# Kernel tuning notes

Hardware: AMD Instinct MI355X
Metric: run time of the kernel (lower is better)

## Reference

```python
import jax, jax.numpy as jnp
import numpy as np

N = 100000      # nodes
E = 800000      # edges (nnz of sparse adj)
D_IN = 128      # input feature dim
H = 64          # hidden_units
EMB = 32        # embsize
N_IDX = 50000   # gathered output rows
EPS = 1e-05     # BatchNormalization epsilon


def spmm(rows, cols, vals, x):
    # out[i] = sum_{e: rows[e]==i} vals[e] * x[cols[e]]  == sparse A @ x
    return jax.ops.segment_sum(vals[:, None] * x[cols], rows, num_segments=N)


def batchnorm(x, gamma, beta):
    # training-mode BN over node (batch) axis, matching Keras BatchNormalization
    m = jnp.mean(x, axis=0)
    v = jnp.var(x, axis=0)
    return (x - m) * jax.lax.rsqrt(v + EPS) * gamma + beta


def setup_inputs() -> dict:
    key = jax.random.key(0)
    ks = jax.random.split(key, 16)
    def w(k, fan_in, shape):
        return jax.random.normal(k, shape, dtype=jnp.float32) / np.sqrt(fan_in)
    inp = {
        "features": jax.random.normal(ks[0], (N, D_IN), dtype=jnp.float32),
        "rows": jax.random.randint(ks[1], (E,), 0, N),
        "cols": jax.random.randint(ks[2], (E,), 0, N),
        "vals": jax.random.uniform(ks[3], (E,), dtype=jnp.float32),
        "idx": jax.random.randint(ks[4], (N_IDX,), 0, N),
        # layer 0 (Dense with bias since l==0)
        "Wn0": w(ks[5], D_IN, (D_IN, H)), "bn0": jnp.zeros((H,), jnp.float32),
        "Wg0": w(ks[6], D_IN, (D_IN, H)), "bg0": jnp.zeros((H,), jnp.float32),
        "ab0": jnp.zeros((H,), jnp.float32),  # BiasLayer after SpMM
        "g0": jnp.ones((H,), jnp.float32), "b0": jnp.zeros((H,), jnp.float32),
        # layer 1 (no Dense bias)
        "Wn1": w(ks[7], H, (H, H)),
        "Wg1": w(ks[8], H, (H, H)),
        "ab1": jnp.zeros((H,), jnp.float32),
        "g1": jnp.ones((H,), jnp.float32), "b1": jnp.zeros((H,), jnp.float32),
        # conv_last block (Dense use_bias=False)
        "WnL": w(ks[9], H, (H, EMB)),
        "WgL": w(ks[10], H, (H, EMB)),
        "abL": jnp.zeros((EMB,), jnp.float32),
    }
    return inp


def reference(features, rows, cols, vals, idx,
              Wn0, bn0, Wg0, bg0, ab0, g0, b0,
              Wn1, Wg1, ab1, g1, b1,
              WnL, WgL, abL):
    x = features
    # SAGE layer 0
    x_node = x @ Wn0 + bn0
    x_neigh = x @ Wg0 + bg0
    agg = spmm(rows, cols, vals, x_neigh) + ab0
    x = jax.nn.relu(batchnorm(x_node + agg, g0, b0))
    # SAGE layer 1
    x_node = x @ Wn1
    x_neigh = x @ Wg1
    agg = spmm(rows, cols, vals, x_neigh) + ab1
    x = jax.nn.relu(batchnorm(x_node + agg, g1, b1))
    # conv_last projection to embsize
    x_node = x @ WnL
    x_neigh = x @ WgL
    agg = spmm(rows, cols, vals, x_neigh) + abL
    x = x_node + agg
    return x[idx]
```

## Files before the change

### kernel.cpp

```cpp
#include <hip/hip_runtime.h>

#define NNODES 100000
#define NEDGES 800000
#define DIN    128
#define HID    64
#define EMB    32
#define NIDX   50000
#define BN_EPS 1e-5f

#define NCHK 256
#define EC   (NEDGES / NCHK)
#define SUBC 256
#define ECS  (NEDGES / SUBC)
#define NB   ((NNODES + 63) / 64)
#define HB   ((NB + 1) / 2)

typedef __attribute__((ext_vector_type(8))) short short8;
typedef __attribute__((ext_vector_type(4))) float f32x4;

__device__ inline unsigned short f2bf(float f) {
    unsigned u = __float_as_uint(f);
    unsigned r = u + 0x7FFFu + ((u >> 16) & 1u);
    return (unsigned short)(r >> 16);
}
__device__ inline float bf2f_lo(unsigned u) { return __uint_as_float(u << 16); }
__device__ inline float bf2f_hi(unsigned u) { return __uint_as_float(u & 0xffff0000u); }


__device__ inline void pack_seg(const float* __restrict__ Wn, const float* __restrict__ Wg,
                                unsigned short* __restrict__ Wp, int HOUT, int l2nt, int f) {
    int j = f & 7, lane = (f >> 3) & 63, g = f >> 9;
    int tt = g & ((1 << l2nt) - 1), kb = g >> l2nt;
    int k = kb * 32 + ((lane >> 4) * 8) + j;
    int nn = tt * 16 + (lane & 15);
    float v = (nn < HOUT) ? Wn[k * HOUT + nn] : Wg[k * HOUT + (nn - HOUT)];
    Wp[f] = f2bf(v);
}


__global__ __launch_bounds__(256) void histpack_k(
    const int* __restrict__ rows, int* __restrict__ Bcnt4,
    const int* __restrict__ idx, int* __restrict__ mark,
    const float* Wn0, const float* Wg0, const float* Wn1,
    const float* Wg1, const float* WnL, const float* WgL,
    unsigned short* Wp0, unsigned short* Wp1, unsigned short* WpL, int MB)
{
    int blk = blockIdx.x;
    if (blk >= SUBC + MB) {
        int f = (blk - SUBC - MB) * 256 + threadIdx.x;
        if (f < 16384)      pack_seg(Wn0, Wg0, Wp0, 64, 3, f);
        else if (f < 24576) pack_seg(Wn1, Wg1, Wp1, 64, 3, f - 16384);
        else if (f < 28672) pack_seg(WnL, WgL, WpL, 32, 2, f - 24576);
        return;
    }
    if (blk >= SUBC) {
        int j = (blk - SUBC) * 256 + threadIdx.x;
        if (j < NIDX) mark[idx[j]] = 1;
        return;
    }
    __shared__ int hist[NB];
    int t = threadIdx.x;
    for (int b = t; b < NB; b += 256) hist[b] = 0;
    __syncthreads();
    for (int i = t; i < ECS; i += 256)
        atomicAdd(&hist[rows[blk * ECS + i] >> 6], 1);
    __syncthreads();
    for (int b = t; b < NB; b += 256) Bcnt4[blk * NB + b] = hist[b];
}

__global__ void bprefix_k(const int* __restrict__ Bcnt4, int* __restrict__ BcntT,
                          int* __restrict__ bTot) {
    int b = blockIdx.x * 256 + threadIdx.x;
    if (b >= NB) return;
    int run = 0;
    for (int sub = 0; sub < SUBC; sub++) {
        BcntT[sub * NB + b] = run;
        run += Bcnt4[sub * NB + b];
    }
    bTot[b] = run;
}

__global__ void bscan_k(const int* __restrict__ bTot, int* __restrict__ bBase) {
    __shared__ int s[256];
    int t = threadIdx.x;
    int v[7], loc = 0;
#pragma unroll
    for (int i = 0; i < 7; i++) {
        int ix = t * 7 + i;
        v[i] = loc;
        loc += (ix < NB) ? bTot[ix] : 0;
    }
    s[t] = loc;
    __syncthreads();
    for (int off = 1; off < 256; off <<= 1) {
        int a = (t >= off) ? s[t - off] : 0;
        __syncthreads();
        s[t] += a;
        __syncthreads();
    }
    int base = s[t] - loc;
#pragma unroll
    for (int i = 0; i < 7; i++) {
        int ix = t * 7 + i;
        if (ix < NB) bBase[ix] = base + v[i];
    }
    if (t == 255) bBase[NB] = NEDGES;
}

__global__ __launch_bounds__(256) void bfinal_k(const uint2* __restrict__ ebuf,
                                                const int* __restrict__ bBase,
                                                int* __restrict__ rowptr,
                                                int2* __restrict__ cs) {
    __shared__ int hist[64], sc[64], cur[64];
    int b = blockIdx.x, t = threadIdx.x;
    int e0 = bBase[b], e1 = bBase[b + 1];
    int r0 = b << 6;
    if (t < 64) hist[t] = 0;
    __syncthreads();
    for (int i = e0 + t; i < e1; i += 256)
        atomicAdd(&hist[(ebuf[i].x >> 20) & 63], 1);
    __syncthreads();
    if (t == 0) {
        int run = e0;
        for (int j = 0; j < 64; j++) { sc[j] = run; run += hist[j]; }
    }
    __syncthreads();
    if (t < 64) {
        cur[t] = sc[t];
        int r = r0 + t;
        if (r < NNODES) rowptr[r] = sc[t];
    }
    if (b == NB - 1 && t == 0) rowptr[NNODES] = NEDGES;
    __syncthreads();
    for (int i = e0 + t; i < e1; i += 256) {
        uint2 v = ebuf[i];
        int p = atomicAdd(&cur[(v.x >> 20) & 63], 1);
        cs[p] = make_int2((int)(v.x & 0xFFFFF), (int)v.y);
    }
}


template <int K, int HOUT, bool AFF, bool XBF, bool HNBF>
__device__ void gemm_body(const void* __restrict__ Xv, const unsigned short* __restrict__ Wp,
                          const float* __restrict__ bnA, const float* __restrict__ bnB,
                          const float* __restrict__ bgA,
                          const float* __restrict__ sums, const float* __restrict__ gamma,
                          const float* __restrict__ beta,
                          float* __restrict__ Hnf, unsigned short* __restrict__ Hnb,
                          unsigned short* __restrict__ Hgb, int n, int blk)
{
    constexpr int NT = 2 * HOUT / 16, NKB = K / 32;
    constexpr int RS = K + 8;
    __shared__ unsigned short Xs[64 * RS];
    __shared__ float sSc[64], sSh[64];

    const int row0 = blk * 64;
    const int t = threadIdx.x;

    if (AFF) {
        if (t < 64) {
            float sum = 0.f, sq = 0.f;
#pragma unroll
            for (int s = 0; s < 8; s++) { sum += sums[s * 128 + t]; sq += sums[s * 128 + 64 + t]; }
            float m = sum / (float)NNODES;
            float var = sq / (float)NNODES - m * m;
            float sc = gamma[t] * rsqrtf(var + BN_EPS);
            sSc[t] = sc; sSh[t] = beta[t] - m * sc;
        }
        __syncthreads();
    }

    for (int li = t; li < 64 * K / 8; li += 256) {
        int r  = li / (K / 8);
        int k8 = (li % (K / 8)) * 8;
        int rr = row0 + r;
        float v[8];
        if (XBF) {
            uint4 u = (rr < n) ? *(const uint4*)((const unsigned short*)Xv + (size_t)rr * K + k8)
                               : make_uint4(0, 0, 0, 0);
            v[0] = bf2f_lo(u.x); v[1] = bf2f_hi(u.x);
            v[2] = bf2f_lo(u.y); v[3] = bf2f_hi(u.y);
            v[4] = bf2f_lo(u.z); v[5] = bf2f_hi(u.z);
            v[6] = bf2f_lo(u.w); v[7] = bf2f_hi(u.w);
        } else {
            const float* Xf = (const float*)Xv;
            float4 a = make_float4(0.f, 0.f, 0.f, 0.f), b = a;
            if (rr < n) {
                a = *(const float4*)&Xf[(size_t)rr * K + k8];
                b = *(const float4*)&Xf[(size_t)rr * K + k8 + 4];
            }
            v[0] = a.x; v[1] = a.y; v[2] = a.z; v[3] = a.w;
            v[4] = b.x; v[5] = b.y; v[6] = b.z; v[7] = b.w;
        }
        if (AFF) {
#pragma unroll
            for (int i = 0; i < 8; i++) v[i] = fmaxf(v[i] * sSc[k8 + i] + sSh[k8 + i], 0.f);
        }
        uint4 o;
        o.x = (unsigned)f2bf(v[0]) | ((unsigned)f2bf(v[1]) << 16);
        o.y = (unsigned)f2bf(v[2]) | ((unsigned)f2bf(v[3]) << 16);
        o.z = (unsigned)f2bf(v[4]) | ((unsigned)f2bf(v[5]) << 16);
        o.w = (unsigned)f2bf(v[6]) | ((unsigned)f2bf(v[7]) << 16);
        *(uint4*)&Xs[r * RS + k8] = o;
    }
    __syncthreads();

    const int wave = t >> 6, lane = t & 63;
    const int q = lane >> 4, mrow = lane & 15;

    f32x4 acc[NT];
#pragma unroll
    for (int i = 0; i < NT; i++) acc[i] = (f32x4){0.f, 0.f, 0.f, 0.f};

    const short8* wp8 = (const short8*)Wp;
#pragma unroll
    for (int kb = 0; kb < NKB; kb++) {
        short8 a = *(const short8*)&Xs[(wave * 16 + mrow) * RS + kb * 32 + q * 8];
#pragma unroll
        for (int tt = 0; tt < NT; tt++) {
            short8 b = wp8[(kb * NT + tt) * 64 + lane];
            acc[tt] = __builtin_amdgcn_mfma_f32_16x16x32_bf16(a, b, acc[tt], 0, 0, 0);
        }
    }

#pragma unroll
    for (int tt = 0; tt < NT; tt++) {
        int nglob = tt * 16 + mrow;
        bool nside = (nglob < HOUT);
        int c = nside ? nglob : (nglob - HOUT);
        float bias = 0.f;
        if (nside) {
            if (bnA) bias += bnA[c];
            if (bnB) bias += bnB[c];
        } else if (bgA) {
            bias += bgA[c];
        }
#pragma unroll
        for (int r = 0; r < 4; r++) {
            int rr = row0 + wave * 16 + q * 4 + r;
            if (rr < n) {
                float o = acc[tt][r] + bias;
                if (nside) {
                    if (HNBF) Hnb[(size_t)rr * HOUT + c] = f2bf(o);
                    else      Hnf[(size_t)rr * HOUT + c] = o;
                } else {
                    Hgb[(size_t)rr * HOUT + c] = f2bf(o);
                }
            }
        }
    }
}

__global__ __launch_bounds__(256) void part_gemm0_k(
    const int* __restrict__ rows, const int* __restrict__ cols,
    const float* __restrict__ vals, const int* __restrict__ BcntT,
    const int* __restrict__ bBase, uint2* __restrict__ ebuf,
    const float* __restrict__ X, const unsigned short* __restrict__ Wp0,
    const float* __restrict__ bn0, const float* __restrict__ ab0, const float* __restrict__ bg0,
    unsigned short* __restrict__ Hn0b, unsigned short* __restrict__ Hgb, int n)
{
    if ((int)blockIdx.x < 2 * NCHK) {
        __shared__ int cur[HB];
        int t = threadIdx.x;
        int blk = blockIdx.x >> 1, half = blockIdx.x & 1;
        int b0 = half * HB, b1 = (half ? NB : HB);
        for (int b = b0 + t; b < b1; b += 256)
            cur[b - b0] = bBase[b] + BcntT[blk * NB + b];
        __syncthreads();
        for (int i = t; i < EC; i += 256) {
            int e = blk * EC + i;
            int r = rows[e];
            int b = r >> 6;
            if (b < b0 || b >= b1) continue;
            int p = atomicAdd(&cur[b - b0], 1);
            ebuf[p] = make_uint2(((unsigned)(r & 63) << 20) | (unsigned)cols[e],
                                 (unsigned)__float_as_int(vals[e]));
        }
    } else {
        gemm_body<DIN, HID, false, false, true>(X, Wp0, bn0, ab0, bg0,
            nullptr, nullptr, nullptr, nullptr, Hn0b, Hgb, n, blockIdx.x - 2 * NCHK);
    }
}

template <int K, int HOUT, bool AFF, bool XBF, bool HNBF>
__global__ __launch_bounds__(256) void gemm_k(
    const void* __restrict__ X, const unsigned short* __restrict__ Wp,
    const float* __restrict__ bnA, const float* __restrict__ bnB, const float* __restrict__ bgA,
    const float* __restrict__ sums, const float* __restrict__ gamma, const float* __restrict__ beta,
    float* __restrict__ Hnf, unsigned short* __restrict__ Hnb, unsigned short* __restrict__ Hgb, int n)
{
    gemm_body<K, HOUT, AFF, XBF, HNBF>(X, Wp, bnA, bnB, bgA, sums, gamma, beta,
                                       Hnf, Hnb, Hgb, n, blockIdx.x);
}


template <int HH, bool STATS, bool SBF, bool MARKED>
__global__ __launch_bounds__(256) void spmm_k(
    const int* __restrict__ rowptr, const int2* __restrict__ cs,
    const unsigned short* __restrict__ Hgb, void* __restrict__ Sv,
    float* __restrict__ stats, const int* __restrict__ mark, int n)
{
    constexpr int L  = HH / 4;
    constexpr int GP = 256 / L;
    const int lane = threadIdx.x % L;
    const int g = threadIdx.x / L;
    const int gid = blockIdx.x * GP + g;
    const int ngroups = gridDim.x * GP;
    const int c0 = lane * 4;

    float4 sum = make_float4(0.f, 0.f, 0.f, 0.f);
    float4 sq  = make_float4(0.f, 0.f, 0.f, 0.f);
    for (int row = gid; row < n; row += ngroups) {
        if (MARKED && !mark[row]) continue;
        int e0 = rowptr[row], e1 = rowptr[row + 1];
        float4 a0, a1, a2, a3;
        if (SBF) {
            uint2 h = *(const uint2*)((const unsigned short*)Sv + (size_t)row * HH + c0);
            a0 = make_float4(bf2f_lo(h.x), bf2f_hi(h.x), bf2f_lo(h.y), bf2f_hi(h.y));
        } else {
            a0 = *(const float4*)((const float*)Sv + (size_t)row * HH + c0);
        }
        a1 = a2 = a3 = make_float4(0.f, 0.f, 0.f, 0.f);
        int e = e0;
        for (; e + 3 < e1; e += 4) {
            int2 p0 = cs[e], p1 = cs[e + 1], p2 = cs[e + 2], p3 = cs[e + 3];
            float v0 = __int_as_float(p0.y), v1 = __int_as_float(p1.y);
            float v2 = __int_as_float(p2.y), v3 = __int_as_float(p3.y);
            uint2 h0 = *(const uint2*)&Hgb[(size_t)p0.x * HH + c0];
            uint2 h1 = *(const uint2*)&Hgb[(size_t)p1.x * HH + c0];
            uint2 h2 = *(const uint2*)&Hgb[(size_t)p2.x * HH + c0];
            uint2 h3 = *(const uint2*)&Hgb[(size_t)p3.x * HH + c0];
            a0.x += v0 * bf2f_lo(h0.x); a0.y += v0 * bf2f_hi(h0.x);
            a0.z += v0 * bf2f_lo(h0.y); a0.w += v0 * bf2f_hi(h0.y);
            a1.x += v1 * bf2f_lo(h1.x); a1.y += v1 * bf2f_hi(h1.x);
            a1.z += v1 * bf2f_lo(h1.y); a1.w += v1 * bf2f_hi(h1.y);
            a2.x += v2 * bf2f_lo(h2.x); a2.y += v2 * bf2f_hi(h2.x);
            a2.z += v2 * bf2f_lo(h2.y); a2.w += v2 * bf2f_hi(h2.y);
            a3.x += v3 * bf2f_lo(h3.x); a3.y += v3 * bf2f_hi(h3.x);
            a3.z += v3 * bf2f_lo(h3.y); a3.w += v3 * bf2f_hi(h3.y);
        }
        for (; e < e1; e++) {
            int2 p = cs[e];
            float v = __int_as_float(p.y);
            uint2 h = *(const uint2*)&Hgb[(size_t)p.x * HH + c0];
            a0.x += v * bf2f_lo(h.x); a0.y += v * bf2f_hi(h.x);
            a0.z += v * bf2f_lo(h.y); a0.w += v * bf2f_hi(h.y);
        }
        float4 acc = make_float4(a0.x + a1.x + a2.x + a3.x, a0.y + a1.y + a2.y + a3.y,
                                 a0.z + a1.z + a2.z + a3.z, a0.w + a1.w + a2.w + a3.w);
        if (SBF) {
            uint2 o;
            o.x = (unsigned)f2bf(acc.x) | ((unsigned)f2bf(acc.y) << 16);
            o.y = (unsigned)f2bf(acc.z) | ((unsigned)f2bf(acc.w) << 16);
            *(uint2*)((unsigned short*)Sv + (size_t)row * HH + c0) = o;
        } else {
            *(float4*)((float*)Sv + (size_t)row * HH + c0) = acc;
        }
        if (STATS) {
            sum.x += acc.x; sum.y += acc.y; sum.z += acc.z; sum.w += acc.w;
            sq.x += acc.x * acc.x; sq.y += acc.y * acc.y;
            sq.z += acc.z * acc.z; sq.w += acc.w * acc.w;
        }
    }

    if constexpr (STATS) {
        __shared__ float rs[GP][HH];
        __shared__ float rq[GP][HH];
        *(float4*)&rs[g][c0] = sum;
        *(float4*)&rq[g][c0] = sq;
        __syncthreads();
        if (threadIdx.x < HH) {
            float a = 0.f, b = 0.f;
            for (int w = 0; w < GP; w++) { a += rs[w][threadIdx.x]; b += rq[w][threadIdx.x]; }
            int stripe = blockIdx.x & 7;
            atomicAdd(&stats[stripe * 128 + threadIdx.x], a);
            atomicAdd(&stats[stripe * 128 + HH + threadIdx.x], b);
        }
    }
}

__global__ void gather_k(const float* __restrict__ S, const int* __restrict__ idx,
                         float* __restrict__ out, int total4) {
    int j = blockIdx.x * 256 + threadIdx.x;
    if (j < total4) {
        int r = j / (EMB / 4), c4 = (j % (EMB / 4)) * 4;
        *(float4*)&out[(size_t)j * 4] = *(const float4*)&S[(size_t)idx[r] * EMB + c4];
    }
}


extern "C" void kernel_launch(void* const* d_in, const int* in_sizes, int n_in,
                              void* d_out, int out_size, void* d_ws, size_t ws_size,
                              hipStream_t stream) {
    const float* features = (const float*)d_in[0];
    const int*   rows     = (const int*)d_in[1];
    const int*   cols     = (const int*)d_in[2];
    const float* vals     = (const float*)d_in[3];
    const int*   idx      = (const int*)d_in[4];
    const float* Wn0 = (const float*)d_in[5];
    const float* bn0 = (const float*)d_in[6];
    const float* Wg0 = (const float*)d_in[7];
    const float* bg0 = (const float*)d_in[8];
    const float* ab0 = (const float*)d_in[9];
    const float* g0  = (const float*)d_in[10];
    const float* b0  = (const float*)d_in[11];
    const float* Wn1 = (const float*)d_in[12];
    const float* Wg1 = (const float*)d_in[13];
    const float* ab1 = (const float*)d_in[14];
    const float* g1  = (const float*)d_in[15];
    const float* b1  = (const float*)d_in[16];
    const float* WnL = (const float*)d_in[17];
    const float* WgL = (const float*)d_in[18];
    const float* abL = (const float*)d_in[19];
    float* out = (float*)d_out;

    float*          HnLf = (float*)d_ws;
    unsigned short* nA   = (unsigned short*)(HnLf + (size_t)NNODES * EMB);
    unsigned short* nB   = nA + (size_t)NNODES * HID;
    unsigned short* Hgb  = nB + (size_t)NNODES * HID;
    uint2* ebuf  = (uint2*)(Hgb + (size_t)NNODES * HID);
    int2*  cs    = (int2*)(ebuf + NEDGES);
    int*   rowptr = (int*)(cs + NEDGES);
    int*   Bcnt4 = rowptr + (NNODES + 4);
    int*   BcntT = Bcnt4 + SUBC * NB;
    int*   bTot  = BcntT + NCHK * NB;
    int*   bBase = bTot + 1568;
    unsigned short* Wp0 = (unsigned short*)(bBase + 1568);
    unsigned short* Wp1 = Wp0 + 16384;
    unsigned short* WpL = Wp1 + 8192;
    float* stats = (float*)(WpL + 4096);
    int*   mark  = (int*)(stats + 2304);
    float* sums0 = stats;
    float* sums1 = stats + 1024;
    size_t zbytes = 2304 * 4 + (size_t)NNODES * 4;

    hipMemsetAsync(stats, 0, zbytes, stream);

    const int GBm = (NNODES + 63) / 64;
    const int MB  = (NIDX + 255) / 256;

    histpack_k<<<SUBC + MB + 112, 256, 0, stream>>>(
        rows, Bcnt4, idx, mark, Wn0, Wg0, Wn1, Wg1, WnL, WgL, Wp0, Wp1, WpL, MB);
    bprefix_k<<<7, 256, 0, stream>>>(Bcnt4, BcntT, bTot);
    bscan_k<<<1, 256, 0, stream>>>(bTot, bBase);
    part_gemm0_k<<<2 * NCHK + GBm, 256, 0, stream>>>(rows, cols, vals, BcntT, bBase, ebuf,
                                                     features, Wp0, bn0, ab0, bg0,
                                                     nA, Hgb, NNODES);
    bfinal_k<<<NB, 256, 0, stream>>>(ebuf, bBase, rowptr, cs);

    spmm_k<HID, true, true, false><<<1600, 256, 0, stream>>>(rowptr, cs, Hgb, nA, sums0, nullptr, NNODES);

    gemm_k<HID, HID, true, true, true><<<GBm, 256, 0, stream>>>(
        nA, Wp1, ab1, nullptr, nullptr, sums0, g0, b0, nullptr, nB, Hgb, NNODES);
    spmm_k<HID, true, true, false><<<1600, 256, 0, stream>>>(rowptr, cs, Hgb, nB, sums1, nullptr, NNODES);

    gemm_k<HID, EMB, true, true, false><<<GBm, 256, 0, stream>>>(
        nB, WpL, abL, nullptr, nullptr, sums1, g1, b1, HnLf, nullptr, Hgb, NNODES);
    spmm_k<EMB, false, false, true><<<1600, 256, 0, stream>>>(rowptr, cs, Hgb, HnLf, nullptr, mark, NNODES);

    gather_k<<<(NIDX * EMB / 4 + 255) / 256, 256, 0, stream>>>(HnLf, idx, out, NIDX * EMB / 4);
}
```

Before: 278.8 us.

## Stage GEMM outputs through LDS for vector stores, batch input loads, fewer partition chunks

The GEMM epilogue now writes bf16 results into shared memory and then stores them to global memory as 16-byte vectors, replacing scattered 2-byte stores. Input tile loads are issued all at once before conversion, using clamped row indices so more memory requests are in flight. The edge-partition chunk count drops from 256 to 64, and the prefix kernel emits offsets only at chunk boundaries. This adds two block barriers and a larger shared buffer, and the coarser partitioning reduces parallelism in the scatter stage.

```diff
diff --git a/kernel.cpp b/kernel.cpp
--- a/kernel.cpp
+++ b/kernel.cpp
@@ -8,10 +8,11 @@
 #define NIDX   50000
 #define BN_EPS 1e-5f
 
-#define NCHK 256
+#define NCHK 64
 #define EC   (NEDGES / NCHK)
 #define SUBC 256
 #define ECS  (NEDGES / SUBC)
+#define SPC  (SUBC / NCHK)
 #define NB   ((NNODES + 63) / 64)
 #define HB   ((NB + 1) / 2)
 
@@ -74,7 +75,8 @@
     if (b >= NB) return;
     int run = 0;
     for (int sub = 0; sub < SUBC; sub++) {
-        BcntT[sub * NB + b] = run;
+        if ((sub & (SPC - 1)) == 0)
+            BcntT[(sub / SPC) * NB + b] = run;
         run += Bcnt4[sub * NB + b];
     }
     bTot[b] = run;
@@ -151,7 +153,10 @@
 {
     constexpr int NT = 2 * HOUT / 16, NKB = K / 32;
     constexpr int RS = K + 8;
-    __shared__ unsigned short Xs[64 * RS];
+    constexpr int OC = HNBF ? 2 * HOUT : HOUT;
+    constexpr int RSE = OC + 8;
+    constexpr int XSZ = (RS > RSE) ? RS : RSE;
+    __shared__ unsigned short Xs[64 * XSZ];
     __shared__ float sSc[64], sSh[64];
 
     const int row0 = blk * 64;
@@ -170,38 +175,68 @@
         __syncthreads();
     }
 
-    for (int li = t; li < 64 * K / 8; li += 256) {
-        int r  = li / (K / 8);
-        int k8 = (li % (K / 8)) * 8;
-        int rr = row0 + r;
-        float v[8];
-        if (XBF) {
-            uint4 u = (rr < n) ? *(const uint4*)((const unsigned short*)Xv + (size_t)rr * K + k8)
-                               : make_uint4(0, 0, 0, 0);
-            v[0] = bf2f_lo(u.x); v[1] = bf2f_hi(u.x);
-            v[2] = bf2f_lo(u.y); v[3] = bf2f_hi(u.y);
-            v[4] = bf2f_lo(u.z); v[5] = bf2f_hi(u.z);
-            v[6] = bf2f_lo(u.w); v[7] = bf2f_hi(u.w);
-        } else {
-            const float* Xf = (const float*)Xv;
-            float4 a = make_float4(0.f, 0.f, 0.f, 0.f), b = a;
-            if (rr < n) {
-                a = *(const float4*)&Xf[(size_t)rr * K + k8];
-                b = *(const float4*)&Xf[(size_t)rr * K + k8 + 4];
+    constexpr int SIT = K / 32;
+    if constexpr (XBF) {
+        uint4 u[SIT];
+#pragma unroll
+        for (int it = 0; it < SIT; it++) {
+            int li = it * 256 + t;
+            int rr = row0 + li / (K / 8);
+            int k8 = (li % (K / 8)) * 8;
+            int rc = rr < n ? rr : n - 1;
+            u[it] = *(const uint4*)((const unsigned short*)Xv + (size_t)rc * K + k8);
+        }
+#pragma unroll
+        for (int it = 0; it < SIT; it++) {
+            int li = it * 256 + t;
+            int r  = li / (K / 8);
+            int k8 = (li % (K / 8)) * 8;
+            float v[8];
+            v[0] = bf2f_lo(u[it].x); v[1] = bf2f_hi(u[it].x);
+            v[2] = bf2f_lo(u[it].y); v[3] = bf2f_hi(u[it].y);
+            v[4] = bf2f_lo(u[it].z); v[5] = bf2f_hi(u[it].z);
+            v[6] = bf2f_lo(u[it].w); v[7] = bf2f_hi(u[it].w);
+            if (AFF) {
+#pragma unroll
+                for (int i = 0; i < 8; i++) v[i] = fmaxf(v[i] * sSc[k8 + i] + sSh[k8 + i], 0.f);
             }
-            v[0] = a.x; v[1] = a.y; v[2] = a.z; v[3] = a.w;
-            v[4] = b.x; v[5] = b.y; v[6] = b.z; v[7] = b.w;
-        }
-        if (AFF) {
-#pragma unroll
-            for (int i = 0; i < 8; i++) v[i] = fmaxf(v[i] * sSc[k8 + i] + sSh[k8 + i], 0.f);
-        }
-        uint4 o;
-        o.x = (unsigned)f2bf(v[0]) | ((unsigned)f2bf(v[1]) << 16);
-        o.y = (unsigned)f2bf(v[2]) | ((unsigned)f2bf(v[3]) << 16);
-        o.z = (unsigned)f2bf(v[4]) | ((unsigned)f2bf(v[5]) << 16);
-        o.w = (unsigned)f2bf(v[6]) | ((unsigned)f2bf(v[7]) << 16);
-        *(uint4*)&Xs[r * RS + k8] = o;
+            uint4 o;
+            o.x = (unsigned)f2bf(v[0]) | ((unsigned)f2bf(v[1]) << 16);
+            o.y = (unsigned)f2bf(v[2]) | ((unsigned)f2bf(v[3]) << 16);
+            o.z = (unsigned)f2bf(v[4]) | ((unsigned)f2bf(v[5]) << 16);
+            o.w = (unsigned)f2bf(v[6]) | ((unsigned)f2bf(v[7]) << 16);
+            *(uint4*)&Xs[r * RS + k8] = o;
+        }
+    } else {
+        const float* Xf = (const float*)Xv;
+        float4 a[SIT], b[SIT];
+#pragma unroll
+        for (int it = 0; it < SIT; it++) {
+            int li = it * 256 + t;
+            int rr = row0 + li / (K / 8);
+            int k8 = (li % (K / 8)) * 8;
+            int rc = rr < n ? rr : n - 1;
+            a[it] = *(const float4*)&Xf[(size_t)rc * K + k8];
+            b[it] = *(const float4*)&Xf[(size_t)rc * K + k8 + 4];
+        }
+#pragma unroll
+        for (int it = 0; it < SIT; it++) {
+            int li = it * 256 + t;
+            int r  = li / (K / 8);
+            int k8 = (li % (K / 8)) * 8;
+            float v[8] = { a[it].x, a[it].y, a[it].z, a[it].w,
+                           b[it].x, b[it].y, b[it].z, b[it].w };
+            if (AFF) {
+#pragma unroll
+                for (int i = 0; i < 8; i++) v[i] = fmaxf(v[i] * sSc[k8 + i] + sSh[k8 + i], 0.f);
+            }
+            uint4 o;
+            o.x = (unsigned)f2bf(v[0]) | ((unsigned)f2bf(v[1]) << 16);
+            o.y = (unsigned)f2bf(v[2]) | ((unsigned)f2bf(v[3]) << 16);
+            o.z = (unsigned)f2bf(v[4]) | ((unsigned)f2bf(v[5]) << 16);
+            o.w = (unsigned)f2bf(v[6]) | ((unsigned)f2bf(v[7]) << 16);
+            *(uint4*)&Xs[r * RS + k8] = o;
+        }
     }
     __syncthreads();
 
@@ -215,14 +250,15 @@
     const short8* wp8 = (const short8*)Wp;
 #pragma unroll
     for (int kb = 0; kb < NKB; kb++) {
-        short8 a = *(const short8*)&Xs[(wave * 16 + mrow) * RS + kb * 32 + q * 8];
+        short8 va = *(const short8*)&Xs[(wave * 16 + mrow) * RS + kb * 32 + q * 8];
 #pragma unroll
         for (int tt = 0; tt < NT; tt++) {
-            short8 b = wp8[(kb * NT + tt) * 64 + lane];
-            acc[tt] = __builtin_amdgcn_mfma_f32_16x16x32_bf16(a, b, acc[tt], 0, 0, 0);
-        }
-    }
-
+            short8 vb = wp8[(kb * NT + tt) * 64 + lane];
+            acc[tt] = __builtin_amdgcn_mfma_f32_16x16x32_bf16(va, vb, acc[tt], 0, 0, 0);
+        }
+    }
+
+    __syncthreads();
 #pragma unroll
     for (int tt = 0; tt < NT; tt++) {
         int nglob = tt * 16 + mrow;
@@ -235,18 +271,33 @@
         } else if (bgA) {
             bias += bgA[c];
         }
-#pragma unroll
-        for (int r = 0; r < 4; r++) {
-            int rr = row0 + wave * 16 + q * 4 + r;
-            if (rr < n) {
-                float o = acc[tt][r] + bias;
-                if (nside) {
-                    if (HNBF) Hnb[(size_t)rr * HOUT + c] = f2bf(o);
-                    else      Hnf[(size_t)rr * HOUT + c] = o;
-                } else {
-                    Hgb[(size_t)rr * HOUT + c] = f2bf(o);
-                }
+        if (HNBF || !nside) {
+            int cc = HNBF ? nglob : c;
+#pragma unroll
+            for (int r = 0; r < 4; r++)
+                Xs[(wave * 16 + q * 4 + r) * RSE + cc] = f2bf(acc[tt][r] + bias);
+        } else {
+#pragma unroll
+            for (int r = 0; r < 4; r++) {
+                int rr = row0 + wave * 16 + q * 4 + r;
+                if (rr < n) Hnf[(size_t)rr * HOUT + c] = acc[tt][r] + bias;
             }
+        }
+    }
+    __syncthreads();
+    constexpr int J = OC / 8;
+#pragma unroll
+    for (int u2 = 0; u2 < (64 * J) / 256; u2++) {
+        int li = u2 * 256 + t;
+        int r = li / J, j = li % J;
+        int rr = row0 + r;
+        if (rr < n) {
+            uint4 v = *(const uint4*)&Xs[r * RSE + j * 8];
+            int c8 = j * 8;
+            if (HNBF && c8 < HOUT)
+                *(uint4*)&Hnb[(size_t)rr * HOUT + c8] = v;
+            else
+                *(uint4*)&Hgb[(size_t)rr * HOUT + (HNBF ? c8 - HOUT : c8)] = v;
         }
     }
 }
```

New measurement: 301.9 us. 8.3% more time.
